# Kernel tuning notes

Hardware: AMD Instinct MI355X
Metric: run time of the kernel (lower is better)

## Reference

```python
import jax, jax.numpy as jnp
import numpy as np

EMBED_DIM = 1024
NUM_HEADS = 16
HEAD_DIM = EMBED_DIM // NUM_HEADS
ROPE_BASE = 10000.0


def setup_inputs() -> dict:
    key = jax.random.key(0)
    ks = jax.random.split(key, 5)
    B, S, D = 2, 2048, EMBED_DIM
    # kaiming_uniform_(a=sqrt(5)) on [out, in] -> bound = 1/sqrt(in)
    bound = 1.0 / np.sqrt(D)
    x = jax.random.normal(ks[0], (B, S, D), dtype=jnp.float32)
    Wq = jax.random.uniform(ks[1], (D, D), dtype=jnp.float32, minval=-bound, maxval=bound)
    Wk = jax.random.uniform(ks[2], (D, D), dtype=jnp.float32, minval=-bound, maxval=bound)
    Wv = jax.random.uniform(ks[3], (D, D), dtype=jnp.float32, minval=-bound, maxval=bound)
    Wo = jax.random.uniform(ks[4], (D, D), dtype=jnp.float32, minval=-bound, maxval=bound)
    return {"x": x, "Wq": Wq, "Wk": Wk, "Wv": Wv, "Wo": Wo}


def _rope(t):
    # t: [B, H, S, hd]; standard half-split RoPE, base 10000
    hd = t.shape[-1]
    half = hd // 2
    S = t.shape[2]
    inv_freq = 1.0 / (ROPE_BASE ** (jnp.arange(half, dtype=jnp.float32) / half))
    ang = jnp.arange(S, dtype=jnp.float32)[:, None] * inv_freq[None, :]  # [S, half]
    cos, sin = jnp.cos(ang), jnp.sin(ang)
    t1, t2 = t[..., :half], t[..., half:]
    return jnp.concatenate([t1 * cos - t2 * sin, t1 * sin + t2 * cos], axis=-1)


def _attention_mc(x, Wq, Wk, Wv, Wo):
    B, S, D = x.shape
    H, hd = NUM_HEADS, HEAD_DIM
    # Linear layers: y = x @ W.T (no bias)
    q = (x @ Wq.T).reshape(B, S, H, hd).transpose(0, 2, 1, 3)  # [B,H,S,hd]
    k = (x @ Wk.T).reshape(B, S, H, hd).transpose(0, 2, 1, 3)
    v = (x @ Wv.T).reshape(B, S, H, hd).transpose(0, 2, 1, 3)
    q = _rope(q)
    k = _rope(k)
    scale = 1.0 / jnp.sqrt(jnp.float32(hd))
    scores = jnp.einsum("bhqd,bhkd->bhqk", q, k) * scale  # [B,H,S,S]
    causal = jnp.tril(jnp.ones((S, S), dtype=bool))
    scores = jnp.where(causal, scores, jnp.finfo(scores.dtype).min)
    attn = jax.nn.softmax(scores, axis=-1)
    out = jnp.einsum("bhqk,bhkd->bhqd", attn, v)  # [B,H,S,hd]
    out = out.transpose(0, 2, 1, 3).reshape(B, S, D)
    return out @ Wo.T


def reference(x, Wq, Wk, Wv, Wo):
    return _attention_mc(x, Wq, Wk, Wv, Wo)
```

## Files before the change

kernel.cpp:

```cpp
#include <hip/hip_runtime.h>
#include <math.h>
#include <stdint.h>


#define S_LEN 2048
#define NHEAD 16
#define HDIM  64
#define NBH   32

typedef __attribute__((ext_vector_type(8))) short  bf16x8;
typedef __attribute__((ext_vector_type(4))) float  f32x4;
typedef unsigned short u16;
typedef unsigned int   u32;

__device__ __forceinline__ u16 f2bf(float f) {
    u32 u = __float_as_uint(f);
    return (u16)((u + 0x7FFFu + ((u >> 16) & 1u)) >> 16);
}
__device__ __forceinline__ float bf2f(u16 s) {
    return __uint_as_float(((u32)s) << 16);
}
__device__ __forceinline__ f32x4 mfma16(bf16x8 a, bf16x8 b, f32x4 c) {
    return __builtin_amdgcn_mfma_f32_16x16x32_bf16(a, b, c, 0, 0, 0);
}

__global__ __launch_bounds__(256)
void split_convert(const float* __restrict__ x,
                   const float* __restrict__ Wq, const float* __restrict__ Wk,
                   const float* __restrict__ Wv, const float* __restrict__ Wo,
                   u16* __restrict__ xhi, u16* __restrict__ xlo,
                   u16* __restrict__ whi, u16* __restrict__ wlo)
{
    const int g = blockIdx.x * 256 + threadIdx.x;
    const float* src; u16 *dhi, *dlo; int loc;
    if (g < 1048576) { src = x; dhi = xhi; dlo = xlo; loc = g; }
    else {
        const int r = g - 1048576;
        const int wsel = r >> 18;
        loc = r & 262143;
        src = (wsel == 0) ? Wq : (wsel == 1) ? Wk : (wsel == 2) ? Wv : Wo;
        dhi = whi + ((size_t)wsel << 20);
        dlo = wlo + ((size_t)wsel << 20);
    }
    const float4 v = reinterpret_cast<const float4*>(src)[loc];
    ushort4 hv, lv;
    hv.x = f2bf(v.x); lv.x = f2bf(v.x - bf2f(hv.x));
    hv.y = f2bf(v.y); lv.y = f2bf(v.y - bf2f(hv.y));
    hv.z = f2bf(v.z); lv.z = f2bf(v.z - bf2f(hv.z));
    hv.w = f2bf(v.w); lv.w = f2bf(v.w - bf2f(hv.w));
    reinterpret_cast<ushort4*>(dhi)[loc] = hv;
    reinterpret_cast<ushort4*>(dlo)[loc] = lv;
}

__global__ __launch_bounds__(256)
void qkv_mfma(const u16* __restrict__ xhi, const u16* __restrict__ xlo,
              const u16* __restrict__ whi, const u16* __restrict__ wlo,
              u16* __restrict__ qhi, u16* __restrict__ qlo,
              u16* __restrict__ khi, u16* __restrict__ klo,
              u16* __restrict__ vthi, u16* __restrict__ vtlo)
{
    __shared__ __align__(16) u16 SMEM[20480];
    const int tid = threadIdx.x, lane = tid & 63, w = tid >> 6;
    const int l15 = lane & 15, l16 = lane >> 4;
    const int lin = blockIdx.y * 32 + blockIdx.x;
    const int xcd = lin & 7, idx = lin >> 3;
    const int nb = xcd * 3 + (idx % 3);
    const int mb = idx / 3;
    const int m0 = mb * 128;
    const int ng = nb * 128;
    const int tsel = ng >> 10;
    const int nloc0 = ng & 1023;
    const u16* __restrict__ Wh = whi + ((size_t)tsel << 20);
    const u16* __restrict__ Wl = wlo + ((size_t)tsel << 20);

    const int r0 = tid >> 2, r1 = r0 + 64;
    const int c0 = (tid & 3) * 8;

    f32x4 acc[4][4];
    #pragma unroll
    for (int i = 0; i < 4; ++i)
        #pragma unroll
        for (int j = 0; j < 4; ++j) acc[i][j] = (f32x4){0.f, 0.f, 0.f, 0.f};

    uint4 Ah0, Ah1, Al0, Al1, Bh0, Bh1, Bl0, Bl1;
    {
        const size_t a0 = (size_t)(m0 + r0) * 1024 + c0;
        const size_t a1 = (size_t)(m0 + r1) * 1024 + c0;
        const size_t b0 = (size_t)(nloc0 + r0) * 1024 + c0;
        const size_t b1 = (size_t)(nloc0 + r1) * 1024 + c0;
        Ah0 = *(const uint4*)&xhi[a0]; Ah1 = *(const uint4*)&xhi[a1];
        Al0 = *(const uint4*)&xlo[a0]; Al1 = *(const uint4*)&xlo[a1];
        Bh0 = *(const uint4*)&Wh[b0];  Bh1 = *(const uint4*)&Wh[b1];
        Bl0 = *(const uint4*)&Wl[b0];  Bl1 = *(const uint4*)&Wl[b1];
    }

    for (int k0 = 0; k0 < 1024; k0 += 32) {
        __syncthreads();
        *(uint4*)&SMEM[        r0 * 32 + c0] = Ah0;
        *(uint4*)&SMEM[        r1 * 32 + c0] = Ah1;
        *(uint4*)&SMEM[ 4096 + r0 * 32 + c0] = Al0;
        *(uint4*)&SMEM[ 4096 + r1 * 32 + c0] = Al1;
        *(uint4*)&SMEM[ 8192 + r0 * 32 + c0] = Bh0;
        *(uint4*)&SMEM[ 8192 + r1 * 32 + c0] = Bh1;
        *(uint4*)&SMEM[12288 + r0 * 32 + c0] = Bl0;
        *(uint4*)&SMEM[12288 + r1 * 32 + c0] = Bl1;
        __syncthreads();
        if (k0 + 32 < 1024) {
            const int kn = k0 + 32;
            const size_t a0 = (size_t)(m0 + r0) * 1024 + kn + c0;
            const size_t a1 = (size_t)(m0 + r1) * 1024 + kn + c0;
            const size_t b0 = (size_t)(nloc0 + r0) * 1024 + kn + c0;
            const size_t b1 = (size_t)(nloc0 + r1) * 1024 + kn + c0;
            Ah0 = *(const uint4*)&xhi[a0]; Ah1 = *(const uint4*)&xhi[a1];
            Al0 = *(const uint4*)&xlo[a0]; Al1 = *(const uint4*)&xlo[a1];
            Bh0 = *(const uint4*)&Wh[b0];  Bh1 = *(const uint4*)&Wh[b1];
            Bl0 = *(const uint4*)&Wl[b0];  Bl1 = *(const uint4*)&Wl[b1];
        }
        const int mo = (w >> 1) * 64, no = (w & 1) * 64;
        bf16x8 a_h[4], a_l[4], b_h[4], b_l[4];
        #pragma unroll
        for (int f = 0; f < 4; ++f) {
            const int ao = (mo + f * 16 + l15) * 32 + l16 * 8;
            a_h[f] = *(const bf16x8*)&SMEM[ao];
            a_l[f] = *(const bf16x8*)&SMEM[4096 + ao];
            const int bo = (no + f * 16 + l15) * 32 + l16 * 8;
            b_h[f] = *(const bf16x8*)&SMEM[8192 + bo];
            b_l[f] = *(const bf16x8*)&SMEM[12288 + bo];
        }
        #pragma unroll
        for (int i = 0; i < 4; ++i)
            #pragma unroll
            for (int j = 0; j < 4; ++j) {
                acc[i][j] = mfma16(a_h[i], b_h[j], acc[i][j]);
                acc[i][j] = mfma16(a_h[i], b_l[j], acc[i][j]);
                acc[i][j] = mfma16(a_l[i], b_h[j], acc[i][j]);
            }
    }

    __syncthreads();
    const int mo = (w >> 1) * 64, no = (w & 1) * 64;
    const int hh = (nloc0 + no) >> 6;
    const int mrow = m0 + mo;
    const int b = mrow >> 11, sb0 = mrow & 2047;
    u16* const chunk = SMEM + w * 5120;

    if (tsel < 2) {
        u16* __restrict__ dh = tsel ? khi : qhi;
        u16* __restrict__ dl = tsel ? klo : qlo;
        const float scl = tsel ? 1.0f : 0.125f;
        const float inv0 = (float)exp((double)l15        * -0.28782313662425574);
        const float inv1 = (float)exp((double)(l15 + 16) * -0.28782313662425574);
        u16* const Thi = chunk;
        u16* const Tlo = chunk + 2304;
        #pragma unroll
        for (int half = 0; half < 2; ++half) {
            #pragma unroll
            for (int i2 = 0; i2 < 2; ++i2) {
                const int i = half * 2 + i2;
                #pragma unroll
                for (int e = 0; e < 4; ++e) {
                    const int rl = i2 * 16 + l16 * 4 + e;
                    const int s = sb0 + half * 32 + rl;
                    #pragma unroll
                    for (int j = 0; j < 2; ++j) {
                        const float inv = j ? inv1 : inv0;
                        const float ang = (float)s * inv;
                        const float sn = sinf(ang), cs = cosf(ang);
                        const float x1 = acc[i][j][e], x2 = acc[i][j + 2][e];
                        const float o1 = (x1 * cs - x2 * sn) * scl;
                        const float o2 = (x1 * sn + x2 * cs) * scl;
                        const u16 h1 = f2bf(o1), h2 = f2bf(o2);
                        Thi[rl * 72 + j * 16 + l15]       = h1;
                        Tlo[rl * 72 + j * 16 + l15]       = f2bf(o1 - bf2f(h1));
                        Thi[rl * 72 + (j + 2) * 16 + l15] = h2;
                        Tlo[rl * 72 + (j + 2) * 16 + l15] = f2bf(o2 - bf2f(h2));
                    }
                }
            }
            #pragma unroll
            for (int p = 0; p < 4; ++p) {
                const int slot = p * 64 + lane;
                const int rr = slot >> 3, c8 = (slot & 7) * 8;
                const size_t ga = (((size_t)(b * NHEAD + hh) * S_LEN) + sb0 + half * 32 + rr) * HDIM + c8;
                *(uint4*)&dh[ga] = *(const uint4*)&Thi[rr * 72 + c8];
                *(uint4*)&dl[ga] = *(const uint4*)&Tlo[rr * 72 + c8];
            }
        }
    } else {
        u16* const Thi = chunk;
        u16* const Tlo = chunk + 2560;
        #pragma unroll
        for (int half = 0; half < 2; ++half) {
            #pragma unroll
            for (int i2 = 0; i2 < 2; ++i2) {
                const int i = half * 2 + i2;
                #pragma unroll
                for (int e = 0; e < 4; ++e) {
                    const int rl = i2 * 16 + l16 * 4 + e;
                    #pragma unroll
                    for (int j = 0; j < 4; ++j) {
                        const float o = acc[i][j][e];
                        const u16 hb = f2bf(o);
                        Thi[(j * 16 + l15) * 40 + rl] = hb;
                        Tlo[(j * 16 + l15) * 40 + rl] = f2bf(o - bf2f(hb));
                    }
                }
            }
            #pragma unroll
            for (int p = 0; p < 4; ++p) {
                const int slot = p * 64 + lane;
                const int dd = slot >> 2, s8 = (slot & 3) * 8;
                const size_t ga = (((size_t)(b * NHEAD + hh) * HDIM) + dd) * S_LEN + sb0 + half * 32 + s8;
                *(uint4*)&vthi[ga] = *(const uint4*)&Thi[dd * 40 + s8];
                *(uint4*)&vtlo[ga] = *(const uint4*)&Tlo[dd * 40 + s8];
            }
        }
    }
}

__global__ __launch_bounds__(256)
void attn_mfma(const u16* __restrict__ qhi, const u16* __restrict__ qlo,
               const u16* __restrict__ khi, const u16* __restrict__ klo,
               const u16* __restrict__ vthi, const u16* __restrict__ vtlo,
               u16* __restrict__ ohi, u16* __restrict__ olo)
{
    __shared__ __align__(16) u16 AS[27136];
    u16* const KH = AS;
    u16* const KL = AS + 4608;
    u16* const VH = AS + 9216;
    u16* const VL = AS + 13824;
    float* const PW = (float*)(AS + 18432);
    const int tid = threadIdx.x, lane = tid & 63, w = tid >> 6;
    const int l15 = lane & 15, l16 = lane >> 4;
    const int lin = blockIdx.y * 32 + blockIdx.x;
    const int xcd = lin & 7, idx = lin >> 3;
    const int bh = xcd * 4 + (idx >> 5);
    const int qt = 31 - (idx & 31);
    const size_t sbase = (size_t)bh * S_LEN * HDIM;
    const size_t dbase = (size_t)bh * HDIM * S_LEN;
    float* const pw = PW + w * 1088;

    bf16x8 q_h[2], q_l[2];
    {
        const int s = qt * 64 + w * 16 + l15;
        #pragma unroll
        for (int ks = 0; ks < 2; ++ks) {
            const size_t ga = sbase + (size_t)s * HDIM + ks * 32 + l16 * 8;
            q_h[ks] = *(const bf16x8*)&qhi[ga];
            q_l[ks] = *(const bf16x8*)&qlo[ga];
        }
    }

    f32x4 oacc[4];
    #pragma unroll
    for (int t = 0; t < 4; ++t) oacc[t] = (f32x4){0.f, 0.f, 0.f, 0.f};
    float m_i[4], l_i[4];
    #pragma unroll
    for (int e = 0; e < 4; ++e) { m_i[e] = -INFINITY; l_i[e] = 0.f; }

    for (int kt = 0; kt <= qt; ++kt) {
        __syncthreads();
        #pragma unroll
        for (int p = 0; p < 2; ++p) {
            const int c = tid + p * 256;
            const int r = c >> 3, dc = (c & 7) * 8;
            const size_t gk = sbase + (size_t)(kt * 64 + r) * HDIM + dc;
            *(uint4*)&KH[r * 72 + dc] = *(const uint4*)&khi[gk];
            *(uint4*)&KL[r * 72 + dc] = *(const uint4*)&klo[gk];
            const size_t gv = dbase + (size_t)r * S_LEN + kt * 64 + dc;
            *(uint4*)&VH[r * 72 + dc] = *(const uint4*)&vthi[gv];
            *(uint4*)&VL[r * 72 + dc] = *(const uint4*)&vtlo[gv];
        }
        __syncthreads();

        f32x4 st[4];
        #pragma unroll
        for (int t = 0; t < 4; ++t) st[t] = (f32x4){0.f, 0.f, 0.f, 0.f};
        #pragma unroll
        for (int t = 0; t < 4; ++t)
            #pragma unroll
            for (int ks = 0; ks < 2; ++ks) {
                const bf16x8 kf_h = *(const bf16x8*)&KH[(t * 16 + l15) * 72 + ks * 32 + l16 * 8];
                const bf16x8 kf_l = *(const bf16x8*)&KL[(t * 16 + l15) * 72 + ks * 32 + l16 * 8];
                st[t] = mfma16(q_h[ks], kf_h, st[t]);
                st[t] = mfma16(q_h[ks], kf_l, st[t]);
                st[t] = mfma16(q_l[ks], kf_h, st[t]);
            }
        if (kt == qt) {
            #pragma unroll
            for (int t = 0; t < 4; ++t)
                #pragma unroll
                for (int e = 0; e < 4; ++e)
                    if (t * 16 + l15 > w * 16 + l16 * 4 + e) st[t][e] = -1e30f;
        }
        #pragma unroll
        for (int e = 0; e < 4; ++e) {
            float mx = fmaxf(fmaxf(st[0][e], st[1][e]), fmaxf(st[2][e], st[3][e]));
            #pragma unroll
            for (int msk = 8; msk >= 1; msk >>= 1) mx = fmaxf(mx, __shfl_xor(mx, msk));
            const float mn = fmaxf(m_i[e], mx);
            const float scl = __expf(m_i[e] - mn);
            float rs = 0.f;
            #pragma unroll
            for (int t = 0; t < 4; ++t) {
                const float p = __expf(st[t][e] - mn);
                st[t][e] = p; rs += p;
            }
            #pragma unroll
            for (int msk = 8; msk >= 1; msk >>= 1) rs += __shfl_xor(rs, msk);
            l_i[e] = l_i[e] * scl + rs;
            m_i[e] = mn;
            #pragma unroll
            for (int t = 0; t < 4; ++t) oacc[t][e] *= scl;
        }
        #pragma unroll
        for (int t = 0; t < 4; ++t)
            #pragma unroll
            for (int e = 0; e < 4; ++e)
                pw[(l16 * 4 + e) * 68 + t * 16 + l15] = st[t][e];
        bf16x8 p_h[2], p_l[2];
        #pragma unroll
        for (int ks = 0; ks < 2; ++ks) {
            float pf[8];
            *(f32x4*)&pf[0] = *(const f32x4*)&pw[l15 * 68 + ks * 32 + l16 * 8];
            *(f32x4*)&pf[4] = *(const f32x4*)&pw[l15 * 68 + ks * 32 + l16 * 8 + 4];
            #pragma unroll
            for (int u = 0; u < 8; ++u) {
                const u16 hb = f2bf(pf[u]);
                p_h[ks][u] = (short)hb;
                p_l[ks][u] = (short)f2bf(pf[u] - bf2f(hb));
            }
        }
        #pragma unroll
        for (int t = 0; t < 4; ++t)
            #pragma unroll
            for (int ks = 0; ks < 2; ++ks) {
                const bf16x8 vf_h = *(const bf16x8*)&VH[(t * 16 + l15) * 72 + ks * 32 + l16 * 8];
                const bf16x8 vf_l = *(const bf16x8*)&VL[(t * 16 + l15) * 72 + ks * 32 + l16 * 8];
                oacc[t] = mfma16(p_h[ks], vf_h, oacc[t]);
                oacc[t] = mfma16(p_h[ks], vf_l, oacc[t]);
                oacc[t] = mfma16(p_l[ks], vf_h, oacc[t]);
            }
    }
    __syncthreads();
    u16* const Ohi = AS + w * 2304;
    u16* const Olo = Ohi + 1152;
    #pragma unroll
    for (int e = 0; e < 4; ++e) {
        const float invl = 1.f / l_i[e];
        const int rl = l16 * 4 + e;
        #pragma unroll
        for (int t = 0; t < 4; ++t) {
            const float o = oacc[t][e] * invl;
            const u16 hb = f2bf(o);
            Ohi[rl * 72 + t * 16 + l15] = hb;
            Olo[rl * 72 + t * 16 + l15] = f2bf(o - bf2f(hb));
        }
    }
    #pragma unroll
    for (int p = 0; p < 2; ++p) {
        const int slot = p * 64 + lane;
        const int rr = slot >> 3, c8 = (slot & 7) * 8;
        const size_t ga = sbase + (size_t)(qt * 64 + w * 16 + rr) * HDIM + c8;
        *(uint4*)&ohi[ga] = *(const uint4*)&Ohi[rr * 72 + c8];
        *(uint4*)&olo[ga] = *(const uint4*)&Olo[rr * 72 + c8];
    }
}

__global__ __launch_bounds__(256)
void proj_mfma(const u16* __restrict__ ahi, const u16* __restrict__ alo,
               const u16* __restrict__ wohi, const u16* __restrict__ wolo,
               float* __restrict__ out)
{
    __shared__ __align__(16) u16 SMEM[16384];
    const int tid = threadIdx.x, lane = tid & 63, w = tid >> 6;
    const int l15 = lane & 15, l16 = lane >> 4;
    const int lin = blockIdx.y * 32 + blockIdx.x;
    const int xcd = lin & 7, idx = lin >> 3;
    const int mb = xcd * 4 + (idx >> 3);
    const int nb = idx & 7;
    const int m0 = mb * 128, n0 = nb * 128;

    const int r0 = tid >> 2, r1 = r0 + 64;
    const int c0 = (tid & 3) * 8;
    const int ri0 = m0 + r0, ri1 = m0 + r1;
    const int ab0 = ri0 >> 11, as0 = ri0 & 2047;
    const int ab1 = ri1 >> 11, as1 = ri1 & 2047;

    f32x4 acc[4][4];
    #pragma unroll
    for (int i = 0; i < 4; ++i)
        #pragma unroll
        for (int j = 0; j < 4; ++j) acc[i][j] = (f32x4){0.f, 0.f, 0.f, 0.f};

    uint4 Ah0, Ah1, Al0, Al1, Bh0, Bh1, Bl0, Bl1;
    {
        const int kc = c0;
        const int hh = kc >> 6, dd = kc & 63;
        const size_t a0 = ((size_t)(ab0 * NHEAD + hh) * S_LEN + as0) * HDIM + dd;
        const size_t a1 = ((size_t)(ab1 * NHEAD + hh) * S_LEN + as1) * HDIM + dd;
        const size_t b0 = (size_t)(n0 + r0) * 1024 + c0;
        const size_t b1 = (size_t)(n0 + r1) * 1024 + c0;
        Ah0 = *(const uint4*)&ahi[a0];  Ah1 = *(const uint4*)&ahi[a1];
        Al0 = *(const uint4*)&alo[a0];  Al1 = *(const uint4*)&alo[a1];
        Bh0 = *(const uint4*)&wohi[b0]; Bh1 = *(const uint4*)&wohi[b1];
        Bl0 = *(const uint4*)&wolo[b0]; Bl1 = *(const uint4*)&wolo[b1];
    }

    for (int k0 = 0; k0 < 1024; k0 += 32) {
        __syncthreads();
        *(uint4*)&SMEM[        r0 * 32 + c0] = Ah0;
        *(uint4*)&SMEM[        r1 * 32 + c0] = Ah1;
        *(uint4*)&SMEM[ 4096 + r0 * 32 + c0] = Al0;
        *(uint4*)&SMEM[ 4096 + r1 * 32 + c0] = Al1;
        *(uint4*)&SMEM[ 8192 + r0 * 32 + c0] = Bh0;
        *(uint4*)&SMEM[ 8192 + r1 * 32 + c0] = Bh1;
        *(uint4*)&SMEM[12288 + r0 * 32 + c0] = Bl0;
        *(uint4*)&SMEM[12288 + r1 * 32 + c0] = Bl1;
        __syncthreads();
        if (k0 + 32 < 1024) {
            const int kc = k0 + 32 + c0;
            const int hh = kc >> 6, dd = kc & 63;
            const size_t a0 = ((size_t)(ab0 * NHEAD + hh) * S_LEN + as0) * HDIM + dd;
            const size_t a1 = ((size_t)(ab1 * NHEAD + hh) * S_LEN + as1) * HDIM + dd;
            const size_t b0 = (size_t)(n0 + r0) * 1024 + k0 + 32 + c0;
            const size_t b1 = (size_t)(n0 + r1) * 1024 + k0 + 32 + c0;
            Ah0 = *(const uint4*)&ahi[a0];  Ah1 = *(const uint4*)&ahi[a1];
            Al0 = *(const uint4*)&alo[a0];  Al1 = *(const uint4*)&alo[a1];
            Bh0 = *(const uint4*)&wohi[b0]; Bh1 = *(const uint4*)&wohi[b1];
            Bl0 = *(const uint4*)&wolo[b0]; Bl1 = *(const uint4*)&wolo[b1];
        }
        const int mo = (w >> 1) * 64, no = (w & 1) * 64;
        bf16x8 a_h[4], a_l[4], b_h[4], b_l[4];
        #pragma unroll
        for (int f = 0; f < 4; ++f) {
            const int ao = (mo + f * 16 + l15) * 32 + l16 * 8;
            a_h[f] = *(const bf16x8*)&SMEM[ao];
            a_l[f] = *(const bf16x8*)&SMEM[4096 + ao];
            const int bo = (no + f * 16 + l15) * 32 + l16 * 8;
            b_h[f] = *(const bf16x8*)&SMEM[8192 + bo];
            b_l[f] = *(const bf16x8*)&SMEM[12288 + bo];
        }
        #pragma unroll
        for (int i = 0; i < 4; ++i)
            #pragma unroll
            for (int j = 0; j < 4; ++j) {
                acc[i][j] = mfma16(a_h[i], b_h[j], acc[i][j]);
                acc[i][j] = mfma16(a_h[i], b_l[j], acc[i][j]);
                acc[i][j] = mfma16(a_l[i], b_h[j], acc[i][j]);
            }
    }
    const int mo = (w >> 1) * 64, no = (w & 1) * 64;
    #pragma unroll
    for (int i = 0; i < 4; ++i)
        #pragma unroll
        for (int e = 0; e < 4; ++e) {
            const int row = m0 + mo + i * 16 + l16 * 4 + e;
            #pragma unroll
            for (int j = 0; j < 4; ++j)
                out[(size_t)row * 1024 + n0 + no + j * 16 + l15] = acc[i][j][e];
        }
}

extern "C" void kernel_launch(void* const* d_in, const int* in_sizes, int n_in,
                              void* d_out, int out_size, void* d_ws, size_t ws_size,
                              hipStream_t stream)
{
    const float* x  = (const float*)d_in[0];
    const float* Wq = (const float*)d_in[1];
    const float* Wk = (const float*)d_in[2];
    const float* Wv = (const float*)d_in[3];
    const float* Wo = (const float*)d_in[4];
    float* out = (float*)d_out;

    char* ws = (char*)d_ws;
    const size_t MB = (size_t)1 << 20;
    u16* xhi  = (u16*)(ws +  0 * MB);
    u16* xlo  = (u16*)(ws +  8 * MB);
    u16* whi  = (u16*)(ws + 16 * MB);
    u16* wlo  = (u16*)(ws + 24 * MB);
    u16* qhi  = (u16*)(ws + 32 * MB);
    u16* qlo  = (u16*)(ws + 40 * MB);
    u16* khi  = (u16*)(ws + 48 * MB);
    u16* klo  = (u16*)(ws + 56 * MB);
    u16* vthi = (u16*)(ws + 64 * MB);
    u16* vtlo = (u16*)(ws + 72 * MB);

    split_convert<<<8192, 256, 0, stream>>>(x, Wq, Wk, Wv, Wo, xhi, xlo, whi, wlo);
    qkv_mfma<<<dim3(32, 24), 256, 0, stream>>>(xhi, xlo, whi, wlo,
                                               qhi, qlo, khi, klo, vthi, vtlo);
    attn_mfma<<<dim3(32, NBH), 256, 0, stream>>>(qhi, qlo, khi, klo, vthi, vtlo,
                                                 xhi, xlo);
    proj_mfma<<<dim3(32, 8), 256, 0, stream>>>(xhi, xlo,
                                               whi + ((size_t)3 << 20), wlo + ((size_t)3 << 20),
                                               out);
}
```

Baseline: 538.8 us.

## Enlarge QKV GEMM tile to 256x256 with 512-thread blocks

The QKV projection kernel moves from 128x128 tiles with 4 waves to 256x256 tiles with 8 waves, each wave computing a 128x64 sub-tile, and LDS grows to 64 KB. The XCD-aware block swizzle is dropped in favour of a plain 12x16 grid, and the RoPE/V-transpose epilogue is reworked to emit 16-row slices. The aim is more operand reuse per LDS load and less global traffic, at the cost of register pressure (128 accumulator floats plus operands), only 192 blocks on the device, and possibly worse L2 locality without the swizzle.

```diff
diff --git a/kernel.cpp b/kernel.cpp
--- a/kernel.cpp
+++ b/kernel.cpp
@@ -52,33 +52,31 @@
     reinterpret_cast<ushort4*>(dlo)[loc] = lv;
 }
 
-__global__ __launch_bounds__(256)
+__global__ __launch_bounds__(512, 2)
 void qkv_mfma(const u16* __restrict__ xhi, const u16* __restrict__ xlo,
               const u16* __restrict__ whi, const u16* __restrict__ wlo,
               u16* __restrict__ qhi, u16* __restrict__ qlo,
               u16* __restrict__ khi, u16* __restrict__ klo,
               u16* __restrict__ vthi, u16* __restrict__ vtlo)
 {
-    __shared__ __align__(16) u16 SMEM[20480];
+    __shared__ __align__(16) u16 SMEM[32768];
     const int tid = threadIdx.x, lane = tid & 63, w = tid >> 6;
     const int l15 = lane & 15, l16 = lane >> 4;
-    const int lin = blockIdx.y * 32 + blockIdx.x;
-    const int xcd = lin & 7, idx = lin >> 3;
-    const int nb = xcd * 3 + (idx % 3);
-    const int mb = idx / 3;
-    const int m0 = mb * 128;
-    const int ng = nb * 128;
-    const int tsel = ng >> 10;
-    const int nloc0 = ng & 1023;
+    const int wr = w >> 2, wc = w & 3;
+    const int nb = blockIdx.x;
+    const int mb = blockIdx.y;
+    const int m0 = mb * 256;
+    const int tsel = nb >> 2;
+    const int nloc0 = (nb & 3) * 256;
     const u16* __restrict__ Wh = whi + ((size_t)tsel << 20);
     const u16* __restrict__ Wl = wlo + ((size_t)tsel << 20);
 
-    const int r0 = tid >> 2, r1 = r0 + 64;
+    const int r0 = tid >> 2, r1 = r0 + 128;
     const int c0 = (tid & 3) * 8;
 
-    f32x4 acc[4][4];
-    #pragma unroll
-    for (int i = 0; i < 4; ++i)
+    f32x4 acc[8][4];
+    #pragma unroll
+    for (int i = 0; i < 8; ++i)
         #pragma unroll
         for (int j = 0; j < 4; ++j) acc[i][j] = (f32x4){0.f, 0.f, 0.f, 0.f};
 
@@ -98,12 +96,12 @@
         __syncthreads();
         *(uint4*)&SMEM[        r0 * 32 + c0] = Ah0;
         *(uint4*)&SMEM[        r1 * 32 + c0] = Ah1;
-        *(uint4*)&SMEM[ 4096 + r0 * 32 + c0] = Al0;
-        *(uint4*)&SMEM[ 4096 + r1 * 32 + c0] = Al1;
-        *(uint4*)&SMEM[ 8192 + r0 * 32 + c0] = Bh0;
-        *(uint4*)&SMEM[ 8192 + r1 * 32 + c0] = Bh1;
-        *(uint4*)&SMEM[12288 + r0 * 32 + c0] = Bl0;
-        *(uint4*)&SMEM[12288 + r1 * 32 + c0] = Bl1;
+        *(uint4*)&SMEM[ 8192 + r0 * 32 + c0] = Al0;
+        *(uint4*)&SMEM[ 8192 + r1 * 32 + c0] = Al1;
+        *(uint4*)&SMEM[16384 + r0 * 32 + c0] = Bh0;
+        *(uint4*)&SMEM[16384 + r1 * 32 + c0] = Bh1;
+        *(uint4*)&SMEM[24576 + r0 * 32 + c0] = Bl0;
+        *(uint4*)&SMEM[24576 + r1 * 32 + c0] = Bl1;
         __syncthreads();
         if (k0 + 32 < 1024) {
             const int kn = k0 + 32;
@@ -116,33 +114,32 @@
             Bh0 = *(const uint4*)&Wh[b0];  Bh1 = *(const uint4*)&Wh[b1];
             Bl0 = *(const uint4*)&Wl[b0];  Bl1 = *(const uint4*)&Wl[b1];
         }
-        const int mo = (w >> 1) * 64, no = (w & 1) * 64;
-        bf16x8 a_h[4], a_l[4], b_h[4], b_l[4];
-        #pragma unroll
-        for (int f = 0; f < 4; ++f) {
-            const int ao = (mo + f * 16 + l15) * 32 + l16 * 8;
-            a_h[f] = *(const bf16x8*)&SMEM[ao];
-            a_l[f] = *(const bf16x8*)&SMEM[4096 + ao];
-            const int bo = (no + f * 16 + l15) * 32 + l16 * 8;
-            b_h[f] = *(const bf16x8*)&SMEM[8192 + bo];
-            b_l[f] = *(const bf16x8*)&SMEM[12288 + bo];
-        }
-        #pragma unroll
-        for (int i = 0; i < 4; ++i)
+        bf16x8 b_h[4], b_l[4];
+        #pragma unroll
+        for (int j = 0; j < 4; ++j) {
+            const int bo = 16384 + (wc * 64 + j * 16 + l15) * 32 + l16 * 8;
+            b_h[j] = *(const bf16x8*)&SMEM[bo];
+            b_l[j] = *(const bf16x8*)&SMEM[bo + 8192];
+        }
+        #pragma unroll
+        for (int i = 0; i < 8; ++i) {
+            const int ao = (wr * 128 + i * 16 + l15) * 32 + l16 * 8;
+            const bf16x8 a_h = *(const bf16x8*)&SMEM[ao];
+            const bf16x8 a_l = *(const bf16x8*)&SMEM[ao + 8192];
             #pragma unroll
             for (int j = 0; j < 4; ++j) {
-                acc[i][j] = mfma16(a_h[i], b_h[j], acc[i][j]);
-                acc[i][j] = mfma16(a_h[i], b_l[j], acc[i][j]);
-                acc[i][j] = mfma16(a_l[i], b_h[j], acc[i][j]);
-            }
+                acc[i][j] = mfma16(a_h, b_h[j], acc[i][j]);
+                acc[i][j] = mfma16(a_h, b_l[j], acc[i][j]);
+                acc[i][j] = mfma16(a_l, b_h[j], acc[i][j]);
+            }
+        }
     }
 
     __syncthreads();
-    const int mo = (w >> 1) * 64, no = (w & 1) * 64;
-    const int hh = (nloc0 + no) >> 6;
-    const int mrow = m0 + mo;
-    const int b = mrow >> 11, sb0 = mrow & 2047;
-    u16* const chunk = SMEM + w * 5120;
+    const int hh = (nb & 3) * 4 + wc;
+    const int m0w = m0 + wr * 128;
+    const int b = m0w >> 11, sb0 = m0w & 2047;
+    u16* const chunk = SMEM + w * 4096;
 
     if (tsel < 2) {
         u16* __restrict__ dh = tsel ? khi : qhi;
@@ -151,68 +148,60 @@
         const float inv0 = (float)exp((double)l15        * -0.28782313662425574);
         const float inv1 = (float)exp((double)(l15 + 16) * -0.28782313662425574);
         u16* const Thi = chunk;
-        u16* const Tlo = chunk + 2304;
-        #pragma unroll
-        for (int half = 0; half < 2; ++half) {
-            #pragma unroll
-            for (int i2 = 0; i2 < 2; ++i2) {
-                const int i = half * 2 + i2;
+        u16* const Tlo = chunk + 1152;
+        #pragma unroll
+        for (int i = 0; i < 8; ++i) {
+            #pragma unroll
+            for (int e = 0; e < 4; ++e) {
+                const int rl = l16 * 4 + e;
+                const int s = sb0 + i * 16 + rl;
                 #pragma unroll
-                for (int e = 0; e < 4; ++e) {
-                    const int rl = i2 * 16 + l16 * 4 + e;
-                    const int s = sb0 + half * 32 + rl;
-                    #pragma unroll
-                    for (int j = 0; j < 2; ++j) {
-                        const float inv = j ? inv1 : inv0;
-                        const float ang = (float)s * inv;
-                        const float sn = sinf(ang), cs = cosf(ang);
-                        const float x1 = acc[i][j][e], x2 = acc[i][j + 2][e];
-                        const float o1 = (x1 * cs - x2 * sn) * scl;
-                        const float o2 = (x1 * sn + x2 * cs) * scl;
-                        const u16 h1 = f2bf(o1), h2 = f2bf(o2);
-                        Thi[rl * 72 + j * 16 + l15]       = h1;
-                        Tlo[rl * 72 + j * 16 + l15]       = f2bf(o1 - bf2f(h1));
-                        Thi[rl * 72 + (j + 2) * 16 + l15] = h2;
-                        Tlo[rl * 72 + (j + 2) * 16 + l15] = f2bf(o2 - bf2f(h2));
-                    }
+                for (int j = 0; j < 2; ++j) {
+                    const float inv = j ? inv1 : inv0;
+                    const float ang = (float)s * inv;
+                    const float sn = sinf(ang), cs = cosf(ang);
+                    const float x1 = acc[i][j][e], x2 = acc[i][j + 2][e];
+                    const float o1 = (x1 * cs - x2 * sn) * scl;
+                    const float o2 = (x1 * sn + x2 * cs) * scl;
+                    const u16 h1 = f2bf(o1), h2 = f2bf(o2);
+                    Thi[rl * 72 + j * 16 + l15]       = h1;
+                    Tlo[rl * 72 + j * 16 + l15]       = f2bf(o1 - bf2f(h1));
+                    Thi[rl * 72 + (j + 2) * 16 + l15] = h2;
+                    Tlo[rl * 72 + (j + 2) * 16 + l15] = f2bf(o2 - bf2f(h2));
                 }
             }
             #pragma unroll
-            for (int p = 0; p < 4; ++p) {
+            for (int p = 0; p < 2; ++p) {
                 const int slot = p * 64 + lane;
                 const int rr = slot >> 3, c8 = (slot & 7) * 8;
-                const size_t ga = (((size_t)(b * NHEAD + hh) * S_LEN) + sb0 + half * 32 + rr) * HDIM + c8;
+                const size_t ga = (((size_t)(b * NHEAD + hh) * S_LEN) + sb0 + i * 16 + rr) * HDIM + c8;
                 *(uint4*)&dh[ga] = *(const uint4*)&Thi[rr * 72 + c8];
                 *(uint4*)&dl[ga] = *(const uint4*)&Tlo[rr * 72 + c8];
             }
         }
     } else {
         u16* const Thi = chunk;
-        u16* const Tlo = chunk + 2560;
-        #pragma unroll
-        for (int half = 0; half < 2; ++half) {
-            #pragma unroll
-            for (int i2 = 0; i2 < 2; ++i2) {
-                const int i = half * 2 + i2;
+        u16* const Tlo = chunk + 1536;
+        #pragma unroll
+        for (int i = 0; i < 8; ++i) {
+            #pragma unroll
+            for (int e = 0; e < 4; ++e) {
+                const int rl = l16 * 4 + e;
                 #pragma unroll
-                for (int e = 0; e < 4; ++e) {
-                    const int rl = i2 * 16 + l16 * 4 + e;
-                    #pragma unroll
-                    for (int j = 0; j < 4; ++j) {
-                        const float o = acc[i][j][e];
-                        const u16 hb = f2bf(o);
-                        Thi[(j * 16 + l15) * 40 + rl] = hb;
-                        Tlo[(j * 16 + l15) * 40 + rl] = f2bf(o - bf2f(hb));
-                    }
+                for (int j = 0; j < 4; ++j) {
+                    const float o = acc[i][j][e];
+                    const u16 hb = f2bf(o);
+                    Thi[(j * 16 + l15) * 24 + rl] = hb;
+                    Tlo[(j * 16 + l15) * 24 + rl] = f2bf(o - bf2f(hb));
                 }
             }
             #pragma unroll
-            for (int p = 0; p < 4; ++p) {
+            for (int p = 0; p < 2; ++p) {
                 const int slot = p * 64 + lane;
-                const int dd = slot >> 2, s8 = (slot & 3) * 8;
-                const size_t ga = (((size_t)(b * NHEAD + hh) * HDIM) + dd) * S_LEN + sb0 + half * 32 + s8;
-                *(uint4*)&vthi[ga] = *(const uint4*)&Thi[dd * 40 + s8];
-                *(uint4*)&vtlo[ga] = *(const uint4*)&Tlo[dd * 40 + s8];
+                const int dd = slot >> 1, s8 = (slot & 1) * 8;
+                const size_t ga = (((size_t)(b * NHEAD + hh) * HDIM) + dd) * S_LEN + sb0 + i * 16 + s8;
+                *(uint4*)&vthi[ga] = *(const uint4*)&Thi[dd * 24 + s8];
+                *(uint4*)&vtlo[ga] = *(const uint4*)&Tlo[dd * 24 + s8];
             }
         }
     }
@@ -487,7 +476,7 @@
     u16* vtlo = (u16*)(ws + 72 * MB);
 
     split_convert<<<8192, 256, 0, stream>>>(x, Wq, Wk, Wv, Wo, xhi, xlo, whi, wlo);
-    qkv_mfma<<<dim3(32, 24), 256, 0, stream>>>(xhi, xlo, whi, wlo,
+    qkv_mfma<<<dim3(12, 16), 512, 0, stream>>>(xhi, xlo, whi, wlo,
                                                qhi, qlo, khi, klo, vthi, vtlo);
     attn_mfma<<<dim3(32, NBH), 256, 0, stream>>>(qhi, qlo, khi, klo, vthi, vtlo,
                                                  xhi, xlo);
```

Result: slower. 585.9 us (+8.7%).
